# Optimization experiments

Hardware: AMD Instinct MI355X
Metric: run time of the kernel (lower is better)

The kernel has to match this reference:

```python
import jax, jax.numpy as jnp
import numpy as np
import math

IN_FEATURES = 4096
OUT_FEATURES = 4096
TOKENS = 8192


def hadamard(x):
    """Orthonormal fast Walsh-Hadamard transform along last dim (power of two)."""
    n = x.shape[-1]
    orig_shape = x.shape
    y = x.reshape(-1, n)
    h = 1
    while h < n:  # log2(n) butterfly steps (static loop, n known at trace time)
        y = y.reshape(-1, n // (2 * h), 2 * h)
        left = y[..., :h]
        right = y[..., h:2 * h]
        y = jnp.concatenate([left + right, left - right], axis=-1)
        y = y.reshape(-1, n)
        h *= 2
    return (y / math.sqrt(n)).reshape(orig_shape)


def setup_inputs() -> dict:
    key = jax.random.key(0)
    k1, k2, k3, k4 = jax.random.split(key, 4)
    x = jax.random.normal(k1, (TOKENS, IN_FEATURES), dtype=jnp.float32)
    # int8-valued quantized weights, stored as int32 for portability
    Q_tilde = jax.random.randint(k2, (OUT_FEATURES, IN_FEATURES), -127, 128, dtype=jnp.int32)
    # per-row scales, positive, realistic magnitude (~max_abs/127)
    s_tilde = jax.random.uniform(k3, (OUT_FEATURES, 1), dtype=jnp.float32, minval=0.001, maxval=0.02)
    bias = jax.random.normal(k4, (OUT_FEATURES,), dtype=jnp.float32)
    return {"x": x, "Q_tilde": Q_tilde, "s_tilde": s_tilde, "bias": bias}


def reference(x, Q_tilde, s_tilde, bias):
    # y = hadamard(x) @ (Q * s)^T + bias
    xh = hadamard(x)                                      # [T, in]
    W = Q_tilde.astype(jnp.float32) * s_tilde             # [out, in] dequantized
    y = xh @ W.T + bias                                   # [T, out]
    return y
```

## Files before the change

### kernel.cpp

```cpp
#include <hip/hip_runtime.h>
#include <hip/hip_bf16.h>

typedef int   i32x4 __attribute__((ext_vector_type(4)));
typedef unsigned int   u32;
typedef unsigned short u16;
typedef signed char    i8;

#define TOKENS 8192
#define NDIM   4096
#define KDIM   4096
#define BK     64
#define NKT    (KDIM / BK)

__global__ __launch_bounds__(64)
void fwht_rows_q8(const float* __restrict__ x, i8* __restrict__ xq,
                  float* __restrict__ xscale) {
  const int row = blockIdx.x;
  const int l   = threadIdx.x;

  const float4* xv = reinterpret_cast<const float4*>(x + (size_t)row * KDIM) + l * 16;
  float v[64];
#pragma unroll
  for (int j = 0; j < 16; ++j) {
    float4 f = xv[j];
    v[4*j+0] = f.x; v[4*j+1] = f.y; v[4*j+2] = f.z; v[4*j+3] = f.w;
  }

#pragma unroll
  for (int h = 1; h < 64; h <<= 1) {
#pragma unroll
    for (int j = 0; j < 64; ++j) {
      if ((j & h) == 0) {
        float a = v[j], b = v[j + h];
        v[j] = a + b; v[j + h] = a - b;
      }
    }
  }

#pragma unroll
  for (int m = 1; m < 64; m <<= 1) {
    const bool up = (l & m) != 0;
#pragma unroll
    for (int j = 0; j < 64; ++j) {
      float p = __shfl_xor(v[j], m, 64);
      v[j] = up ? (p - v[j]) : (v[j] + p);
    }
  }

  float mxu = 0.f;
#pragma unroll
  for (int j = 0; j < 64; ++j) mxu = fmaxf(mxu, fabsf(v[j]));
#pragma unroll
  for (int m = 1; m < 64; m <<= 1) mxu = fmaxf(mxu, __shfl_xor(mxu, m, 64));
  mxu = fmaxf(mxu, 1e-30f);
  const float inv = 127.0f / mxu;

  i8* orow = xq + (size_t)row * KDIM + l * 64;
#pragma unroll
  for (int g = 0; g < 4; ++g) {
    u32 w[4];
#pragma unroll
    for (int q4 = 0; q4 < 4; ++q4) {
      int b0 = __float2int_rn(v[g*16+q4*4+0] * inv);
      int b1 = __float2int_rn(v[g*16+q4*4+1] * inv);
      int b2 = __float2int_rn(v[g*16+q4*4+2] * inv);
      int b3 = __float2int_rn(v[g*16+q4*4+3] * inv);
      b0 = min(127, max(-127, b0)); b1 = min(127, max(-127, b1));
      b2 = min(127, max(-127, b2)); b3 = min(127, max(-127, b3));
      w[q4] = (u32)(b0 & 0xff) | ((u32)(b1 & 0xff) << 8) |
              ((u32)(b2 & 0xff) << 16) | ((u32)(b3 & 0xff) << 24);
    }
    uint4 pk; pk.x = w[0]; pk.y = w[1]; pk.z = w[2]; pk.w = w[3];
    *reinterpret_cast<uint4*>(orow + g * 16) = pk;
  }
  if (l == 0) xscale[row] = mxu * (0.015625f / 127.0f);
}

__device__ __forceinline__ u32 pack4(int4 q) {
  return (u32)(q.x & 0xff) | ((u32)(q.y & 0xff) << 8) |
         ((u32)(q.z & 0xff) << 16) | ((u32)(q.w & 0xff) << 24);
}
__global__ __launch_bounds__(256)
void qpack(const int* __restrict__ Q, i8* __restrict__ W8) {
  const size_t idx = ((size_t)blockIdx.x * 256 + threadIdx.x) * 16;
  int4 a = *reinterpret_cast<const int4*>(Q + idx);
  int4 b = *reinterpret_cast<const int4*>(Q + idx + 4);
  int4 c = *reinterpret_cast<const int4*>(Q + idx + 8);
  int4 d = *reinterpret_cast<const int4*>(Q + idx + 12);
  uint4 pk; pk.x = pack4(a); pk.y = pack4(b); pk.z = pack4(c); pk.w = pack4(d);
  *reinterpret_cast<uint4*>(W8 + idx) = pk;
}

__global__ __launch_bounds__(512, 2)
void gemm256_i8(const i8* __restrict__ A, const i8* __restrict__ B,
                const float* __restrict__ xscale, const float* __restrict__ s,
                const float* __restrict__ bias, float* __restrict__ C) {
  __shared__ __align__(16) i8 lds[4 * 32768];

  const int th   = threadIdx.x;
  const int wave = th >> 6;
  const int lane = th & 63;

  const int b0 = blockIdx.x;
  const int xc = b0 & 7;
  const int i  = b0 >> 3;
  const int mt = i >> 1;
  const int nt = xc * 2 + (i & 1);

  const int srow = th >> 2;
  const int scol = ((th & 3) * 16) ^ (((th >> 5) & 1) << 5);
  const i8* gA0 = A + (size_t)(mt * 256 + srow) * KDIM + scol;
  const i8* gA1 = gA0 + (size_t)128 * KDIM;
  const i8* gB0 = B + (size_t)(nt * 256 + srow) * KDIM + scol;
  const i8* gB1 = gB0 + (size_t)128 * KDIM;

  const int ldsA0 = wave * 1024;
  const int ldsA1 = 8192 + wave * 1024;
  const int ldsB0 = 16384 + wave * 1024;
  const int ldsB1 = 24576 + wave * 1024;

#define STAGE_A(tt, ss) do {                                                    \
    __builtin_amdgcn_global_load_lds(                                           \
      (const __attribute__((address_space(1))) void*)(gA0 + (size_t)(tt) * BK), \
      (__attribute__((address_space(3))) void*)(lds + (ss) * 32768 + ldsA0), 16, 0, 0); \
    __builtin_amdgcn_global_load_lds(                                           \
      (const __attribute__((address_space(1))) void*)(gA1 + (size_t)(tt) * BK), \
      (__attribute__((address_space(3))) void*)(lds + (ss) * 32768 + ldsA1), 16, 0, 0); \
  } while (0)
#define STAGE_B(tt, ss) do {                                                    \
    __builtin_amdgcn_global_load_lds(                                           \
      (const __attribute__((address_space(1))) void*)(gB0 + (size_t)(tt) * BK), \
      (__attribute__((address_space(3))) void*)(lds + (ss) * 32768 + ldsB0), 16, 0, 0); \
    __builtin_amdgcn_global_load_lds(                                           \
      (const __attribute__((address_space(1))) void*)(gB1 + (size_t)(tt) * BK), \
      (__attribute__((address_space(3))) void*)(lds + (ss) * 32768 + ldsB1), 16, 0, 0); \
  } while (0)

  const int wm = wave >> 2;
  const int wn = wave & 3;
  const int laneRow = lane & 15;
  const int kByte   = (lane >> 4) << 4;
  const int swz     = ((lane >> 3) & 1) << 5;
  const int aOff = (((wm * 128 + laneRow) * 64 + kByte) ^ swz);
  const int bOff = (((wn * 64 + laneRow) * 64 + kByte) ^ swz) + 16384;

  i32x4 acc[8][4];
#pragma unroll
  for (int mi = 0; mi < 8; ++mi)
#pragma unroll
    for (int ni = 0; ni < 4; ++ni)
      acc[mi][ni] = i32x4{0, 0, 0, 0};

  STAGE_A(0, 0); STAGE_B(0, 0);
  STAGE_A(1, 1); STAGE_B(1, 1);
  asm volatile("s_waitcnt vmcnt(4)" ::: "memory");
  __builtin_amdgcn_s_barrier();

  for (int t = 0; t < NKT; ++t) {
    const int slot = t & 3;
    const char* base = (const char*)lds + slot * 32768;

    i32x4 bfr[4], af[4];
#pragma unroll
    for (int ni = 0; ni < 4; ++ni)
      bfr[ni] = *(const i32x4*)(base + bOff + ni * 1024);
#pragma unroll
    for (int mi = 0; mi < 4; ++mi)
      af[mi] = *(const i32x4*)(base + aOff + mi * 1024);
    if (t + 2 < NKT) STAGE_A(t + 2, (t + 2) & 3);
    __builtin_amdgcn_s_barrier();
    __builtin_amdgcn_s_setprio(1);
#pragma unroll
    for (int mi = 0; mi < 4; ++mi)
#pragma unroll
      for (int ni = 0; ni < 4; ++ni)
        acc[mi][ni] = __builtin_amdgcn_mfma_i32_16x16x64_i8(af[mi], bfr[ni], acc[mi][ni], 0, 0, 0);
    __builtin_amdgcn_s_setprio(0);
    __builtin_amdgcn_s_barrier();

#pragma unroll
    for (int mi = 0; mi < 4; ++mi)
      af[mi] = *(const i32x4*)(base + aOff + 4096 + mi * 1024);
    if (t + 2 < NKT) STAGE_B(t + 2, (t + 2) & 3);
    __builtin_amdgcn_s_barrier();
    __builtin_amdgcn_s_setprio(1);
#pragma unroll
    for (int mi = 0; mi < 4; ++mi)
#pragma unroll
      for (int ni = 0; ni < 4; ++ni)
        acc[mi + 4][ni] = __builtin_amdgcn_mfma_i32_16x16x64_i8(af[mi], bfr[ni], acc[mi + 4][ni], 0, 0, 0);
    __builtin_amdgcn_s_setprio(0);

    if (t + 2 < NKT)      asm volatile("s_waitcnt vmcnt(4)" ::: "memory");
    else if (t + 1 < NKT) asm volatile("s_waitcnt vmcnt(0)" ::: "memory");
    __builtin_amdgcn_s_barrier();
  }

  const int col0 = nt * 256 + wn * 64 + (lane & 15);
  const int row0 = mt * 256 + wm * 128 + ((lane >> 4) << 2);
  float xs[4][8];
#pragma unroll
  for (int mi = 0; mi < 8; ++mi)
#pragma unroll
    for (int r = 0; r < 4; ++r)
      xs[r][mi] = xscale[row0 + mi * 16 + r];
#pragma unroll
  for (int ni = 0; ni < 4; ++ni) {
    const float sc = s[col0 + ni * 16];
    const float bv = bias[col0 + ni * 16];
#pragma unroll
    for (int mi = 0; mi < 8; ++mi) {
      float* cp = C + (size_t)(row0 + mi * 16) * NDIM + col0 + ni * 16;
#pragma unroll
      for (int r = 0; r < 4; ++r)
        cp[(size_t)r * NDIM] = (float)acc[mi][ni][r] * (xs[r][mi] * sc) + bv;
    }
  }
#undef STAGE_A
#undef STAGE_B
}

extern "C" void kernel_launch(void* const* d_in, const int* in_sizes, int n_in,
                              void* d_out, int out_size, void* d_ws, size_t ws_size,
                              hipStream_t stream) {
  (void)in_sizes; (void)n_in; (void)out_size; (void)ws_size;
  const float* x    = (const float*)d_in[0];
  const int*   Q    = (const int*)d_in[1];
  const float* s    = (const float*)d_in[2];
  const float* bias = (const float*)d_in[3];
  float* out = (float*)d_out;

  i8*    xq     = (i8*)d_ws;
  i8*    W8     = xq + (size_t)TOKENS * KDIM;
  float* xscale = (float*)(W8 + (size_t)NDIM * KDIM);

  fwht_rows_q8<<<dim3(TOKENS), dim3(64), 0, stream>>>(x, xq, xscale);
  qpack<<<dim3((NDIM * KDIM) / (256 * 16)), dim3(256), 0, stream>>>(Q, W8);
  gemm256_i8<<<dim3((TOKENS / 256) * (NDIM / 256)), dim3(512), 0, stream>>>(
      xq, W8, xscale, s, bias, out);
}
```

Baseline: 204.8 us.

## Software-pipeline int8 GEMM loop with register double-buffered fragments and fewer barriers

The GEMM main loop is unrolled by two and B fragments are double-buffered in registers. The next tile's A and B fragments are read from LDS while the current tile's second MFMA half runs. Explicit lgkmcnt/vmcnt waits and sched_barriers replace most of the per-tile s_barriers, going from three per tile to one. The goal is to hide LDS read latency and barrier stalls behind MFMA work. In exchange it uses more VGPRs and depends on hand-counted waitcnt values being correct.

```diff
diff --git a/kernel.cpp b/kernel.cpp
--- a/kernel.cpp
+++ b/kernel.cpp
@@ -154,47 +154,73 @@
   STAGE_A(0, 0); STAGE_B(0, 0);
   STAGE_A(1, 1); STAGE_B(1, 1);
   asm volatile("s_waitcnt vmcnt(4)" ::: "memory");
+  __builtin_amdgcn_sched_barrier(0);
   __builtin_amdgcn_s_barrier();
 
-  for (int t = 0; t < NKT; ++t) {
-    const int slot = t & 3;
-    const char* base = (const char*)lds + slot * 32768;
-
-    i32x4 bfr[4], af[4];
+  i32x4 afA[4], afB[4], bf0[4], bf1[4];
+  {
+    const char* c0 = (const char*)lds;
 #pragma unroll
     for (int ni = 0; ni < 4; ++ni)
-      bfr[ni] = *(const i32x4*)(base + bOff + ni * 1024);
+      bf0[ni] = *(const i32x4*)(c0 + bOff + ni * 1024);
 #pragma unroll
     for (int mi = 0; mi < 4; ++mi)
-      af[mi] = *(const i32x4*)(base + aOff + mi * 1024);
-    if (t + 2 < NKT) STAGE_A(t + 2, (t + 2) & 3);
-    __builtin_amdgcn_s_barrier();
-    __builtin_amdgcn_s_setprio(1);
-#pragma unroll
-    for (int mi = 0; mi < 4; ++mi)
-#pragma unroll
-      for (int ni = 0; ni < 4; ++ni)
-        acc[mi][ni] = __builtin_amdgcn_mfma_i32_16x16x64_i8(af[mi], bfr[ni], acc[mi][ni], 0, 0, 0);
-    __builtin_amdgcn_s_setprio(0);
-    __builtin_amdgcn_s_barrier();
-
-#pragma unroll
-    for (int mi = 0; mi < 4; ++mi)
-      af[mi] = *(const i32x4*)(base + aOff + 4096 + mi * 1024);
-    if (t + 2 < NKT) STAGE_B(t + 2, (t + 2) & 3);
-    __builtin_amdgcn_s_barrier();
-    __builtin_amdgcn_s_setprio(1);
-#pragma unroll
-    for (int mi = 0; mi < 4; ++mi)
-#pragma unroll
-      for (int ni = 0; ni < 4; ++ni)
-        acc[mi + 4][ni] = __builtin_amdgcn_mfma_i32_16x16x64_i8(af[mi], bfr[ni], acc[mi + 4][ni], 0, 0, 0);
-    __builtin_amdgcn_s_setprio(0);
-
-    if (t + 2 < NKT)      asm volatile("s_waitcnt vmcnt(4)" ::: "memory");
-    else if (t + 1 < NKT) asm volatile("s_waitcnt vmcnt(0)" ::: "memory");
-    __builtin_amdgcn_s_barrier();
-  }
+      afA[mi] = *(const i32x4*)(c0 + aOff + mi * 1024);
+  }
+
+#define TILE(t, BFC, BFN) do {                                                  \
+    const char* cur = (const char*)lds + ((t) & 3) * 32768;                     \
+    const char* nxt = (const char*)lds + (((t) + 1) & 3) * 32768;               \
+                              \
+    _Pragma("unroll")                                                           \
+    for (int mi = 0; mi < 4; ++mi)                                              \
+      afB[mi] = *(const i32x4*)(cur + aOff + 4096 + mi * 1024);                 \
+    if ((t) + 2 < NKT) STAGE_A((t) + 2, ((t) + 2) & 3);                         \
+    asm volatile("s_waitcnt lgkmcnt(4)" ::: "memory");       \
+    __builtin_amdgcn_sched_barrier(0);                                          \
+    __builtin_amdgcn_s_setprio(1);                                              \
+    _Pragma("unroll")                                                           \
+    for (int mi = 0; mi < 4; ++mi)                                              \
+      _Pragma("unroll")                                                         \
+      for (int ni = 0; ni < 4; ++ni)                                            \
+        acc[mi][ni] = __builtin_amdgcn_mfma_i32_16x16x64_i8(afA[mi], BFC[ni],   \
+                                                            acc[mi][ni], 0, 0, 0); \
+    __builtin_amdgcn_s_setprio(0);                                              \
+    if ((t) + 1 < NKT) {                                                        \
+      if ((t) + 2 < NKT) { asm volatile("s_waitcnt vmcnt(2)" ::: "memory"); }   \
+      else               { asm volatile("s_waitcnt vmcnt(0)" ::: "memory"); }   \
+      __builtin_amdgcn_sched_barrier(0);                                        \
+      __builtin_amdgcn_s_barrier();          \
+      _Pragma("unroll")                                                         \
+      for (int ni = 0; ni < 4; ++ni)                                            \
+        BFN[ni] = *(const i32x4*)(nxt + bOff + ni * 1024);                      \
+      _Pragma("unroll")                                                         \
+      for (int mi = 0; mi < 4; ++mi)                                            \
+        afA[mi] = *(const i32x4*)(nxt + aOff + mi * 1024);                      \
+      if ((t) + 2 < NKT) STAGE_B((t) + 2, ((t) + 2) & 3);                       \
+      asm volatile("s_waitcnt lgkmcnt(8)" ::: "memory");         \
+      __builtin_amdgcn_sched_barrier(0);                                        \
+    } else {                                                                    \
+      asm volatile("s_waitcnt lgkmcnt(0)" ::: "memory");                        \
+      __builtin_amdgcn_sched_barrier(0);                                        \
+    }                                                                           \
+    __builtin_amdgcn_s_setprio(1);                                              \
+    _Pragma("unroll")                                                           \
+    for (int mi = 0; mi < 4; ++mi)                                              \
+      _Pragma("unroll")                                                         \
+      for (int ni = 0; ni < 4; ++ni)                                            \
+        acc[mi + 4][ni] = __builtin_amdgcn_mfma_i32_16x16x64_i8(afB[mi], BFC[ni], \
+                                                            acc[mi + 4][ni], 0, 0, 0); \
+    __builtin_amdgcn_s_setprio(0);                                              \
+  } while (0)
+
+  for (int t = 0; t < NKT; t += 2) {
+    TILE(t,     bf0, bf1);
+    TILE(t + 1, bf1, bf0);
+  }
+#undef TILE
+#undef STAGE_A
+#undef STAGE_B
 
   const int col0 = nt * 256 + wn * 64 + (lane & 15);
   const int row0 = mt * 256 + wm * 128 + ((lane >> 4) << 2);
@@ -216,8 +242,6 @@
         cp[(size_t)r * NDIM] = (float)acc[mi][ni][r] * (xs[r][mi] * sc) + bv;
     }
   }
-#undef STAGE_A
-#undef STAGE_B
 }
 
 extern "C" void kernel_launch(void* const* d_in, const int* in_sizes, int n_in,
```

Result: no change. 204.7 us (-0.0%).

## Shrink GEMM tile to 256x128 with double-buffered LDS and higher occupancy

Applied to the files above, without the earlier changes.

Changes the int8 GEMM tile from 256x256 to 256x128, with a 4x2 wave layout where each wave computes 64x64. The LDS ring drops from four stages to two, and the kernel requests 4 blocks per CU instead of 2. The aim is to hide latency through more resident blocks rather than deep prefetch. In exchange, arithmetic intensity per tile falls, global traffic for A doubles, and each iteration waits on vmcnt(0) right after the MFMAs, so overlap inside a block is shallower.

```diff
diff --git a/kernel.cpp b/kernel.cpp
--- a/kernel.cpp
+++ b/kernel.cpp
@@ -91,11 +91,11 @@
   *reinterpret_cast<uint4*>(W8 + idx) = pk;
 }
 
-__global__ __launch_bounds__(512, 2)
-void gemm256_i8(const i8* __restrict__ A, const i8* __restrict__ B,
+__global__ __launch_bounds__(512, 4)
+void gemm_i8_2b(const i8* __restrict__ A, const i8* __restrict__ B,
                 const float* __restrict__ xscale, const float* __restrict__ s,
                 const float* __restrict__ bias, float* __restrict__ C) {
-  __shared__ __align__(16) i8 lds[4 * 32768];
+  __shared__ __align__(16) i8 lds[2 * 24576];
 
   const int th   = threadIdx.x;
   const int wave = th >> 6;
@@ -104,71 +104,62 @@
   const int b0 = blockIdx.x;
   const int xc = b0 & 7;
   const int i  = b0 >> 3;
-  const int mt = i >> 1;
-  const int nt = xc * 2 + (i & 1);
+  const int mt = i >> 2;
+  const int nt = xc * 4 + (i & 3);
 
   const int srow = th >> 2;
   const int scol = ((th & 3) * 16) ^ (((th >> 5) & 1) << 5);
   const i8* gA0 = A + (size_t)(mt * 256 + srow) * KDIM + scol;
   const i8* gA1 = gA0 + (size_t)128 * KDIM;
-  const i8* gB0 = B + (size_t)(nt * 256 + srow) * KDIM + scol;
-  const i8* gB1 = gB0 + (size_t)128 * KDIM;
+  const i8* gB0 = B + (size_t)(nt * 128 + srow) * KDIM + scol;
 
   const int ldsA0 = wave * 1024;
   const int ldsA1 = 8192 + wave * 1024;
   const int ldsB0 = 16384 + wave * 1024;
-  const int ldsB1 = 24576 + wave * 1024;
-
-#define STAGE_A(tt, ss) do {                                                    \
+
+#define STAGE(tt, ss) do {                                                      \
     __builtin_amdgcn_global_load_lds(                                           \
       (const __attribute__((address_space(1))) void*)(gA0 + (size_t)(tt) * BK), \
-      (__attribute__((address_space(3))) void*)(lds + (ss) * 32768 + ldsA0), 16, 0, 0); \
+      (__attribute__((address_space(3))) void*)(lds + (ss) * 24576 + ldsA0), 16, 0, 0); \
     __builtin_amdgcn_global_load_lds(                                           \
       (const __attribute__((address_space(1))) void*)(gA1 + (size_t)(tt) * BK), \
-      (__attribute__((address_space(3))) void*)(lds + (ss) * 32768 + ldsA1), 16, 0, 0); \
-  } while (0)
-#define STAGE_B(tt, ss) do {                                                    \
+      (__attribute__((address_space(3))) void*)(lds + (ss) * 24576 + ldsA1), 16, 0, 0); \
     __builtin_amdgcn_global_load_lds(                                           \
       (const __attribute__((address_space(1))) void*)(gB0 + (size_t)(tt) * BK), \
-      (__attribute__((address_space(3))) void*)(lds + (ss) * 32768 + ldsB0), 16, 0, 0); \
-    __builtin_amdgcn_global_load_lds(                                           \
-      (const __attribute__((address_space(1))) void*)(gB1 + (size_t)(tt) * BK), \
-      (__attribute__((address_space(3))) void*)(lds + (ss) * 32768 + ldsB1), 16, 0, 0); \
+      (__attribute__((address_space(3))) void*)(lds + (ss) * 24576 + ldsB0), 16, 0, 0); \
   } while (0)
 
-  const int wm = wave >> 2;
-  const int wn = wave & 3;
+  const int wm = wave >> 1;
+  const int wn = wave & 1;
   const int laneRow = lane & 15;
   const int kByte   = (lane >> 4) << 4;
   const int swz     = ((lane >> 3) & 1) << 5;
-  const int aOff = (((wm * 128 + laneRow) * 64 + kByte) ^ swz);
+  const int aOff = (((wm * 64 + laneRow) * 64 + kByte) ^ swz);
   const int bOff = (((wn * 64 + laneRow) * 64 + kByte) ^ swz) + 16384;
 
-  i32x4 acc[8][4];
-#pragma unroll
-  for (int mi = 0; mi < 8; ++mi)
+  i32x4 acc[4][4];
+#pragma unroll
+  for (int mi = 0; mi < 4; ++mi)
 #pragma unroll
     for (int ni = 0; ni < 4; ++ni)
       acc[mi][ni] = i32x4{0, 0, 0, 0};
 
-  STAGE_A(0, 0); STAGE_B(0, 0);
-  STAGE_A(1, 1); STAGE_B(1, 1);
-  asm volatile("s_waitcnt vmcnt(4)" ::: "memory");
+  STAGE(0, 0);
+  asm volatile("s_waitcnt vmcnt(0)" ::: "memory");
   __builtin_amdgcn_s_barrier();
 
   for (int t = 0; t < NKT; ++t) {
-    const int slot = t & 3;
-    const char* base = (const char*)lds + slot * 32768;
+    const char* cur = (const char*)lds + (t & 1) * 24576;
+    if (t + 1 < NKT) STAGE(t + 1, (t + 1) & 1);
 
     i32x4 bfr[4], af[4];
 #pragma unroll
     for (int ni = 0; ni < 4; ++ni)
-      bfr[ni] = *(const i32x4*)(base + bOff + ni * 1024);
+      bfr[ni] = *(const i32x4*)(cur + bOff + ni * 1024);
 #pragma unroll
     for (int mi = 0; mi < 4; ++mi)
-      af[mi] = *(const i32x4*)(base + aOff + mi * 1024);
-    if (t + 2 < NKT) STAGE_A(t + 2, (t + 2) & 3);
-    __builtin_amdgcn_s_barrier();
+      af[mi] = *(const i32x4*)(cur + aOff + mi * 1024);
+
     __builtin_amdgcn_s_setprio(1);
 #pragma unroll
     for (int mi = 0; mi < 4; ++mi)
@@ -176,31 +167,17 @@
       for (int ni = 0; ni < 4; ++ni)
         acc[mi][ni] = __builtin_amdgcn_mfma_i32_16x16x64_i8(af[mi], bfr[ni], acc[mi][ni], 0, 0, 0);
     __builtin_amdgcn_s_setprio(0);
+
+    asm volatile("s_waitcnt vmcnt(0)" ::: "memory");
     __builtin_amdgcn_s_barrier();
-
-#pragma unroll
-    for (int mi = 0; mi < 4; ++mi)
-      af[mi] = *(const i32x4*)(base + aOff + 4096 + mi * 1024);
-    if (t + 2 < NKT) STAGE_B(t + 2, (t + 2) & 3);
-    __builtin_amdgcn_s_barrier();
-    __builtin_amdgcn_s_setprio(1);
-#pragma unroll
-    for (int mi = 0; mi < 4; ++mi)
-#pragma unroll
-      for (int ni = 0; ni < 4; ++ni)
-        acc[mi + 4][ni] = __builtin_amdgcn_mfma_i32_16x16x64_i8(af[mi], bfr[ni], acc[mi + 4][ni], 0, 0, 0);
-    __builtin_amdgcn_s_setprio(0);
-
-    if (t + 2 < NKT)      asm volatile("s_waitcnt vmcnt(4)" ::: "memory");
-    else if (t + 1 < NKT) asm volatile("s_waitcnt vmcnt(0)" ::: "memory");
-    __builtin_amdgcn_s_barrier();
-  }
-
-  const int col0 = nt * 256 + wn * 64 + (lane & 15);
-  const int row0 = mt * 256 + wm * 128 + ((lane >> 4) << 2);
-  float xs[4][8];
-#pragma unroll
-  for (int mi = 0; mi < 8; ++mi)
+  }
+#undef STAGE
+
+  const int col0 = nt * 128 + wn * 64 + (lane & 15);
+  const int row0 = mt * 256 + wm * 64 + ((lane >> 4) << 2);
+  float xs[4][4];
+#pragma unroll
+  for (int mi = 0; mi < 4; ++mi)
 #pragma unroll
     for (int r = 0; r < 4; ++r)
       xs[r][mi] = xscale[row0 + mi * 16 + r];
@@ -209,15 +186,13 @@
     const float sc = s[col0 + ni * 16];
     const float bv = bias[col0 + ni * 16];
 #pragma unroll
-    for (int mi = 0; mi < 8; ++mi) {
+    for (int mi = 0; mi < 4; ++mi) {
       float* cp = C + (size_t)(row0 + mi * 16) * NDIM + col0 + ni * 16;
 #pragma unroll
       for (int r = 0; r < 4; ++r)
         cp[(size_t)r * NDIM] = (float)acc[mi][ni][r] * (xs[r][mi] * sc) + bv;
     }
   }
-#undef STAGE_A
-#undef STAGE_B
 }
 
 extern "C" void kernel_launch(void* const* d_in, const int* in_sizes, int n_in,
@@ -236,6 +211,6 @@
 
   fwht_rows_q8<<<dim3(TOKENS), dim3(64), 0, stream>>>(x, xq, xscale);
   qpack<<<dim3((NDIM * KDIM) / (256 * 16)), dim3(256), 0, stream>>>(Q, W8);
-  gemm256_i8<<<dim3((TOKENS / 256) * (NDIM / 256)), dim3(512), 0, stream>>>(
+  gemm_i8_2b<<<dim3((TOKENS / 256) * (NDIM / 128)), dim3(512), 0, stream>>>(
       xq, W8, xscale, s, bias, out);
 }
```

Result: slower. 219.4 us (+7.1%).
